# Kernel tuning notes

Hardware: AMD Instinct MI355X
Metric: run time of the kernel (lower is better)

The kernel has to match this reference:

```python
import jax, jax.numpy as jnp
import numpy as np

KAPPA = 0.5  # decorrelation loss mixing coefficient (init kwarg)


def setup_inputs() -> dict:
    key = jax.random.key(0)
    kx, kw, kb, kd, ki = jax.random.split(key, 5)
    b, l, d = 4, 8192, 1024
    n_samples = int(0.25 * l)  # sample_frac = 0.25
    x = jax.random.normal(kx, (b, l, d), dtype=jnp.float32)
    W = jax.random.normal(kw, (d, d), dtype=jnp.float32) * 0.02
    bias = jax.random.normal(kb, (d,), dtype=jnp.float32) * 0.02
    # decorr_layer is initialized at identity in the module; perturb slightly so the
    # decorrelation matmul is non-trivial (it gets updated during training).
    decorr = jnp.eye(d, dtype=jnp.float32) + 0.01 * jax.random.normal(kd, (d, d), dtype=jnp.float32)
    sample_idx = jax.random.randint(ki, (b, n_samples), 0, l)  # stand-in for torch.multinomial
    return {"x": x, "W": W, "bias": bias, "decorr": decorr, "sample_idx": sample_idx}


def reference(x, W, bias, decorr, sample_idx):
    # Output path: y = x @ (W @ decorr)^T + bias
    y = jnp.einsum('bld,od->blo', x, W @ decorr) + bias

    b, l, d = x.shape
    # Gather sampled tokens: [b, n, d]
    selected = jnp.take_along_axis(x, sample_idx[:, :, None], axis=1)
    xs = (selected @ decorr.T).reshape(-1, d)  # [N, d], N = b*n_samples
    N = xs.shape[0]

    # DecorrLoss, algebraically reduced (same math as diag_embed/outer-product form):
    #   C_n = x_n x_n^T - diag(x_n^2)  (zero diagonal, off-diag x_i x_j)
    #   V_n = diag(x_n^2) - I          (diagonal x_i^2 - 1, zero off-diag)
    X2 = xs * xs                     # [N, d]
    m2 = jnp.mean(X2, axis=0)        # [d], mean of x_i^2
    S = X2.T @ X2                    # [d, d]; S_ij = sum_n x_ni^2 x_nj^2
    denom = jnp.float32(N) * d * d
    correlation_loss = (jnp.sum(S) - jnp.trace(S)) / denom       # mean_n mean_ij C_n^2
    whitening_loss = jnp.sum((X2 - 1.0) ** 2) / denom             # mean_n mean_ij V_n^2

    G = (xs.T @ xs) / N              # mean_n x_n x_n^T
    C_mean = G - jnp.diag(m2)
    V_mean = jnp.diag(m2) - jnp.eye(d, dtype=xs.dtype)
    grad = (1.0 - KAPPA) * C_mean + KAPPA * V_mean

    return y, grad, correlation_loss, whitening_loss
```

## Files before the change

### kernel.cpp

```cpp
#include <hip/hip_runtime.h>
#include <cstdint>
#include <cstddef>

typedef __bf16 bf16x8 __attribute__((ext_vector_type(8)));
typedef float  f32x4  __attribute__((ext_vector_type(4)));
typedef unsigned short u16x4 __attribute__((ext_vector_type(4)));

typedef __attribute__((address_space(1))) void* gas1_t;
typedef __attribute__((address_space(3))) void* las3_t;

__device__ __forceinline__ unsigned short f2bf(float f) {
  union { float f; unsigned u; } v; v.f = f;
  unsigned r = v.u + 0x7fffu + ((v.u >> 16) & 1u);
  return (unsigned short)(r >> 16);
}
__device__ __forceinline__ float bf2f(unsigned short h) {
  union { unsigned u; float f; } v; v.u = ((unsigned)h) << 16;
  return v.f;
}

constexpr int Bc = 4, Lc = 8192, Dc = 1024, NSAMP = 2048;
constexpr int ROWS = Bc * Lc;
constexpr int NSEL = Bc * NSAMP;
constexpr long long Y_ELEMS = (long long)ROWS * Dc;
constexpr long long GRAD_OFF = Y_ELEMS;
constexpr long long LOSS_OFF = GRAD_OFF + (long long)Dc*Dc;

constexpr int BM = 128, BN = 128, BK = 64;

template<int MODE>
__global__ void gemm_bt(const unsigned short* __restrict__ A,
                        const unsigned short* __restrict__ B,
                        float* __restrict__ Cf,
                        const float* __restrict__ bias,
                        int M, int N, int K, int kchunk) {
  __shared__ unsigned short sA[BM * BK];
  __shared__ unsigned short sB[BN * BK];
  const int tid  = threadIdx.x;
  const int lane = tid & 63;
  const int wave = tid >> 6;
  const int wm = wave >> 1, wn = wave & 1;
  const int q = lane >> 4, r16 = lane & 15;

  const int gx   = gridDim.x;
  const int nwg  = gx * gridDim.y;
  const int orig = blockIdx.y * gx + blockIdx.x;
  const int swz  = (orig & 7) * (nwg >> 3) + (orig >> 3);
  const int m0 = (swz / gx) * BM;
  const int n0 = (swz % gx) * BN;
  const int kb = blockIdx.z * kchunk;

  const int lrow = lane >> 3;
  const int lcol = (lane & 7) * 8;

  f32x4 acc[4][4] = {};

  for (int k0 = kb; k0 < kb + kchunk; k0 += BK) {
#pragma unroll
    for (int j = 0; j < 4; ++j) {
      const int c = wave * 4 + j;
      const int row = c * 8 + lrow;
      const unsigned short* ga = A + (size_t)(m0 + row) * K + k0 + lcol;
      __builtin_amdgcn_global_load_lds((gas1_t)(void*)ga, (las3_t)(sA + c * 512), 16, 0, 0);
      const unsigned short* gb = B + (size_t)(n0 + row) * K + k0 + lcol;
      __builtin_amdgcn_global_load_lds((gas1_t)(void*)gb, (las3_t)(sB + c * 512), 16, 0, 0);
    }
    __syncthreads();
#pragma unroll
    for (int kk = 0; kk < BK; kk += 32) {
      bf16x8 af[4], bfv[4];
#pragma unroll
      for (int mi = 0; mi < 4; ++mi)
        af[mi] = *(const bf16x8*)(sA + (size_t)(wm*64 + mi*16 + r16) * BK + kk + q*8);
#pragma unroll
      for (int ni = 0; ni < 4; ++ni)
        bfv[ni] = *(const bf16x8*)(sB + (size_t)(wn*64 + ni*16 + r16) * BK + kk + q*8);
#pragma unroll
      for (int mi = 0; mi < 4; ++mi)
#pragma unroll
        for (int ni = 0; ni < 4; ++ni)
          acc[mi][ni] = __builtin_amdgcn_mfma_f32_16x16x32_bf16(af[mi], bfv[ni], acc[mi][ni], 0, 0, 0);
    }
    __syncthreads();
  }

  const int row0 = m0 + wm*64 + q*4;
  const int col0 = n0 + wn*64 + r16;
  float bv[4] = {0.f, 0.f, 0.f, 0.f};
  if (MODE == 0) {
#pragma unroll
    for (int ni = 0; ni < 4; ++ni) bv[ni] = bias[col0 + ni*16];
  }
#pragma unroll
  for (int mi = 0; mi < 4; ++mi) {
#pragma unroll
    for (int r = 0; r < 4; ++r) {
      const int row = row0 + mi*16 + r;
      const size_t base = (size_t)row * N + col0;
#pragma unroll
      for (int ni = 0; ni < 4; ++ni) {
        const size_t o = base + (size_t)ni * 16;
        float v = acc[mi][ni][r];
        if (MODE == 0)      __builtin_nontemporal_store(v + bv[ni], &Cf[o]);
        else if (MODE == 2) Cf[o] = v;
        else                atomicAdd(&Cf[o], v);
      }
    }
  }
}

template<int NT>
__global__ void cvt_f32_bf16(const float* __restrict__ in, unsigned short* __restrict__ out, long long n) {
  long long i = ((long long)blockIdx.x * 256 + threadIdx.x) * 4;
  if (i >= n) return;
  f32x4 v;
  if (NT) v = __builtin_nontemporal_load((const f32x4*)(in + i));
  else    v = *(const f32x4*)(in + i);
  u16x4 o;
  o.x = f2bf(v.x); o.y = f2bf(v.y); o.z = f2bf(v.z); o.w = f2bf(v.w);
  *(u16x4*)(out + i) = o;
}

__global__ void gather_rows(const unsigned short* __restrict__ xb, const int* __restrict__ idx,
                            unsigned short* __restrict__ out) {
  const int blk = blockIdx.x;
  const int b = blk >> 11, n = blk & 2047;
  const int row = idx[b * NSAMP + n];
  const unsigned short* src = xb + ((size_t)b * Lc + row) * Dc;
  unsigned short* dst = out + (size_t)blk * Dc;
  const int c = threadIdx.x * 4;
  *(u16x4*)(dst + c) = *(const u16x4*)(src + c);
}

__global__ void diag_resid(const float* __restrict__ dc, float* __restrict__ cvec) {
  const int i = blockIdx.x * 256 + threadIdx.x;
  if (i >= Dc) return;
  const float v = dc[(size_t)i * Dc + i];
  cvec[i] = v - bf2f(f2bf(v));
}

__global__ void transpose_bf16(const float* __restrict__ in, unsigned short* __restrict__ outT,
                               int R, int C) {
  __shared__ float tile[64][65];
  const int r0 = blockIdx.y * 64, c0 = blockIdx.x * 64;
  const int t = threadIdx.x;
  const int c = t & 63, r4 = t >> 6;
#pragma unroll
  for (int j = 0; j < 16; ++j) {
    const int r = j * 4 + r4;
    tile[r][c] = in[(size_t)(r0 + r) * C + c0 + c];
  }
  __syncthreads();
  const int i = t >> 2, p = t & 3;
  unsigned short* dst = outT + (size_t)(c0 + i) * R + r0 + p * 16;
#pragma unroll
  for (int j = 0; j < 16; j += 4) {
    u16x4 v;
    v.x = f2bf(tile[p*16 + j + 0][i]);
    v.y = f2bf(tile[p*16 + j + 1][i]);
    v.z = f2bf(tile[p*16 + j + 2][i]);
    v.w = f2bf(tile[p*16 + j + 3][i]);
    *(u16x4*)(dst + j) = v;
  }
}

__global__ void xs_stats_transpose(const float* __restrict__ xs, const unsigned short* __restrict__ ab,
                                   const float* __restrict__ cvec,
                                   unsigned short* __restrict__ xsT,
                                   float* __restrict__ m2sum, float* __restrict__ s1g,
                                   float* __restrict__ s2g) {
  __shared__ float tile[64][65];
  const int n0 = blockIdx.x * 64;
  const int i0 = blockIdx.y * 64;
  const int t = threadIdx.x;
  const int c = t & 63, r4 = t >> 6;
  const float ccol = cvec[i0 + c];
#pragma unroll
  for (int j = 0; j < 16; ++j) {
    const int r = j * 4 + r4;
    const size_t o = (size_t)(n0 + r) * Dc + i0 + c;
    tile[r][c] = xs[o] + bf2f(ab[o]) * ccol;
  }
  __syncthreads();
  if (t < 64) {
    float s1 = 0.f, s2 = 0.f;
#pragma unroll
    for (int cc = 0; cc < 64; ++cc) { float v = tile[t][cc]; float v2 = v*v; s1 += v2; s2 += v2*v2; }
    atomicAdd(&s1g[n0 + t], s1);
    atomicAdd(&s2g[n0 + t], s2);
  } else if (t < 128) {
    const int col = t - 64;
    float cs = 0.f;
#pragma unroll
    for (int rr = 0; rr < 64; ++rr) { float v = tile[rr][col]; cs += v*v; }
    atomicAdd(&m2sum[i0 + col], cs);
  }
  const int i = t >> 2, p = t & 3;
  unsigned short* dst = xsT + (size_t)(i0 + i) * NSEL + n0 + p * 16;
#pragma unroll
  for (int j = 0; j < 16; j += 4) {
    u16x4 v;
    v.x = f2bf(tile[p*16 + j + 0][i]);
    v.y = f2bf(tile[p*16 + j + 1][i]);
    v.z = f2bf(tile[p*16 + j + 2][i]);
    v.w = f2bf(tile[p*16 + j + 3][i]);
    *(u16x4*)(dst + j) = v;
  }
}

__global__ void grad_write(const float* __restrict__ G, const float* __restrict__ m2sum,
                           float* __restrict__ out) {
  const int i = blockIdx.x * 256 + threadIdx.x;
  const int r = i >> 10, c = i & 1023;
  float g = G[i] * (0.5f / (float)NSEL);
  if (r == c) g = 0.5f * (m2sum[r] * (1.0f / (float)NSEL) - 1.0f);
  __builtin_nontemporal_store(g, &out[i]);
}

__global__ void finalize_losses(const float* __restrict__ s1g, const float* __restrict__ s2g,
                                float* __restrict__ out2) {
  __shared__ double sa[256], sb[256], sc[256];
  double a = 0, b = 0, c = 0;
  for (int n = threadIdx.x; n < NSEL; n += 256) {
    double s1 = s1g[n], s2 = s2g[n];
    a += s1 * s1; b += s2; c += s1;
  }
  const int t = threadIdx.x;
  sa[t] = a; sb[t] = b; sc[t] = c;
  __syncthreads();
  for (int s = 128; s > 0; s >>= 1) {
    if (t < s) { sa[t] += sa[t+s]; sb[t] += sb[t+s]; sc[t] += sc[t+s]; }
    __syncthreads();
  }
  if (t == 0) {
    const double denom = (double)NSEL * (double)Dc * (double)Dc;
    const double cnt   = (double)NSEL * (double)Dc;
    out2[0] = (float)((sa[0] - sb[0]) / denom);
    out2[1] = (float)((sb[0] - 2.0 * sc[0] + cnt) / denom);
  }
}

extern "C" void kernel_launch(void* const* d_in, const int* in_sizes, int n_in,
                              void* d_out, int out_size, void* d_ws, size_t ws_size,
                              hipStream_t stream) {
  const float* x      = (const float*)d_in[0];
  const float* W      = (const float*)d_in[1];
  const float* bias   = (const float*)d_in[2];
  const float* decorr = (const float*)d_in[3];
  const int*   sidx   = (const int*)d_in[4];
  float* out = (float*)d_out;

  char* w = (char*)d_ws;
  constexpr size_t SZ_XB  = (size_t)ROWS * Dc * 2;
  constexpr size_t SZ_AB  = (size_t)NSEL * Dc * 2;
  constexpr size_t SZ_DT  = (size_t)Dc * Dc * 2;
  constexpr size_t SZ_WB  = (size_t)Dc * Dc * 2;
  constexpr size_t SZ_MB  = (size_t)Dc * Dc * 2;
  constexpr size_t SZ_XS  = (size_t)NSEL * Dc * 4;
  constexpr size_t SZ_XST = (size_t)Dc * NSEL * 2;
  constexpr size_t SZ_MF  = (size_t)Dc * Dc * 4;
  constexpr size_t SZ_GB  = (size_t)Dc * Dc * 4;
  constexpr size_t SZ_M2  = (size_t)Dc * 4;
  constexpr size_t SZ_S1  = (size_t)NSEL * 4;
  constexpr size_t SZ_S2  = (size_t)NSEL * 4;
  constexpr size_t SZ_CV  = (size_t)Dc * 4;

  size_t off = 0;
  unsigned short* xb  = (unsigned short*)(w + off); off += SZ_XB;
  unsigned short* ab  = (unsigned short*)(w + off); off += SZ_AB;
  unsigned short* dT  = (unsigned short*)(w + off); off += SZ_DT;
  unsigned short* wb  = (unsigned short*)(w + off); off += SZ_WB;
  unsigned short* mb  = (unsigned short*)(w + off); off += SZ_MB;
  float*          xsf = (float*)(w + off);          off += SZ_XS;
  unsigned short* xsT = (unsigned short*)(w + off); off += SZ_XST;
  float*          cv  = (float*)(w + off);          off += SZ_CV;
  char*           zbase = w + off;
  float*          Mf  = (float*)(w + off);          off += SZ_MF;
  float*          Gb  = (float*)(w + off);          off += SZ_GB;
  float*          m2s = (float*)(w + off);          off += SZ_M2;
  float*          s1g = (float*)(w + off);          off += SZ_S1;
  float*          s2g = (float*)(w + off);          off += SZ_S2;
  const size_t zbytes = SZ_MF + SZ_GB + SZ_M2 + SZ_S1 + SZ_S2;

  (void)hipMemsetAsync(zbase, 0, zbytes, stream);

  cvt_f32_bf16<1><<<(int)(Y_ELEMS / 1024), 256, 0, stream>>>(x, xb, Y_ELEMS);
  cvt_f32_bf16<0><<<Dc*Dc / 1024, 256, 0, stream>>>(W, wb, (long long)Dc*Dc);
  diag_resid<<<4, 256, 0, stream>>>(decorr, cv);
  transpose_bf16<<<dim3(Dc/64, Dc/64), 256, 0, stream>>>(decorr, dT, Dc, Dc);
  gather_rows<<<NSEL, 256, 0, stream>>>(xb, sidx, ab);

  gemm_bt<3><<<dim3(Dc/BN, Dc/BM, 8), 256, 0, stream>>>(wb, dT, Mf, nullptr, Dc, Dc, Dc, Dc/8);
  cvt_f32_bf16<0><<<Dc*Dc / 1024, 256, 0, stream>>>(Mf, mb, (long long)Dc*Dc);

  gemm_bt<0><<<dim3(Dc/BN, ROWS/BM, 1), 256, 0, stream>>>(xb, mb, out, bias, ROWS, Dc, Dc, Dc);

  gemm_bt<2><<<dim3(Dc/BN, NSEL/BM, 1), 256, 0, stream>>>(ab, dT, xsf, nullptr, NSEL, Dc, Dc, Dc);

  xs_stats_transpose<<<dim3(NSEL/64, Dc/64), 256, 0, stream>>>(xsf, ab, cv, xsT, m2s, s1g, s2g);

  gemm_bt<3><<<dim3(Dc/BN, Dc/BM, 16), 256, 0, stream>>>(xsT, xsT, Gb, nullptr, Dc, Dc, NSEL, NSEL/16);

  grad_write<<<Dc*Dc / 256, 256, 0, stream>>>(Gb, m2s, out + GRAD_OFF);
  finalize_losses<<<1, 256, 0, stream>>>(s1g, s2g, out + LOSS_OFF);
}
```

Before: 470.7 us.

## Add 256x256 direct-to-LDS pipelined GEMM for output and sample projections

Adds a new 512-thread GEMM kernel with 256x256 output tiles. It stages A and B into double-buffered LDS with global_load_lds and splits each K-step into four phases that interleave loads with MFMA bursts under raised wave priority. The main y projection and the sampled-token projection now use this kernel instead of the 128x128 one. The aim is more data reuse per tile and better overlap of memory loads with matrix-core work. In exchange it uses more LDS and registers per block and depends on hand-placed vmcnt waits, and the prologue issues one redundant stage load.

```diff
diff --git a/kernel.cpp b/kernel.cpp
--- a/kernel.cpp
+++ b/kernel.cpp
@@ -25,6 +25,169 @@
 constexpr long long Y_ELEMS = (long long)ROWS * Dc;
 constexpr long long GRAD_OFF = Y_ELEMS;
 constexpr long long LOSS_OFF = GRAD_OFF + (long long)Dc*Dc;
+
+constexpr int BM8 = 256, BN8 = 256;
+
+__device__ __forceinline__ void stage_half(const unsigned short* __restrict__ G,
+                                           unsigned short* lds_half,
+                                           int row0, int K, long long kbase,
+                                           int wave, int srow) {
+#pragma unroll
+  for (int j = 0; j < 2; ++j) {
+    const int w = wave * 2 + j;
+    const unsigned short* src = G + (size_t)(row0 + w * 16 + srow) * K + kbase;
+    __builtin_amdgcn_global_load_lds((gas1_t)(void*)src,
+                                     (las3_t)(lds_half + w * 512), 16, 0, 0);
+  }
+}
+
+__device__ __forceinline__ void ld4(const unsigned short* base, int l8, bf16x8* dst) {
+#pragma unroll
+  for (int i = 0; i < 4; ++i)
+    dst[i] = *(const bf16x8*)(base + i * 512 + l8);
+}
+
+#define PH_WAIT() do {                                        \
+    __builtin_amdgcn_s_barrier();                             \
+    asm volatile("s_waitcnt lgkmcnt(0)" ::: "memory");        \
+    __builtin_amdgcn_sched_barrier(0);                        \
+  } while (0)
+
+template<int MODE>
+__global__ __launch_bounds__(512, 2)
+void gemm_bt8(const unsigned short* __restrict__ A,
+              const unsigned short* __restrict__ B,
+              float* __restrict__ Cf,
+              const float* __restrict__ bias,
+              int M, int N, int K) {
+  __shared__ unsigned short sA[2 * 16384];
+  __shared__ unsigned short sB[2 * 16384];
+  const int tid  = threadIdx.x;
+  const int lane = tid & 63;
+  const int wave = tid >> 6;
+  const int wm = wave >> 2;
+  const int wn = wave & 3;
+  const int q = lane >> 4, r16 = lane & 15;
+  const int l8 = lane * 8;
+  const int srow = lane & 15;
+  const long long scol = (lane >> 4) * 8;
+
+  const int gx   = gridDim.x;
+  const int nwg  = gx * gridDim.y;
+  const int orig = blockIdx.y * gx + blockIdx.x;
+  const int swz  = (orig & 7) * (nwg >> 3) + (orig >> 3);
+  const int m0 = (swz / gx) * BM8;
+  const int n0 = (swz % gx) * BN8;
+
+  const int nt = K >> 6;
+
+  f32x4 acc[8][4] = {};
+
+  {
+    stage_half(A, sA + 0 * 16384 + 0 * 8192, m0, K, 0,            wave, srow ? srow : srow);
+  }
+  stage_half(A, sA + 0,          m0, K, 0 * 64 + 0 * 32 + scol, wave, srow);
+  stage_half(A, sA + 8192,       m0, K, 0 * 64 + 1 * 32 + scol, wave, srow);
+  stage_half(B, sB + 0,          n0, K, 0 * 64 + 0 * 32 + scol, wave, srow);
+  stage_half(B, sB + 8192,       n0, K, 0 * 64 + 1 * 32 + scol, wave, srow);
+  if (nt > 1) {
+    stage_half(B, sB + 16384 + 0,    n0, K, 1 * 64 + 0 * 32 + scol, wave, srow);
+    stage_half(A, sA + 16384 + 0,    m0, K, 1 * 64 + 0 * 32 + scol, wave, srow);
+    stage_half(B, sB + 16384 + 8192, n0, K, 1 * 64 + 1 * 32 + scol, wave, srow);
+    asm volatile("s_waitcnt vmcnt(6)" ::: "memory");
+  } else {
+    asm volatile("s_waitcnt vmcnt(0)" ::: "memory");
+  }
+  __builtin_amdgcn_s_barrier();
+
+  for (int g = 0; g < nt; ++g) {
+    const int buf = (g & 1) * 16384;
+    const int nbuf = 16384 - buf;
+    bf16x8 af[4], bfv[4];
+
+    ld4(sA + buf + (wm * 8 + 0) * 512, l8, af);
+    ld4(sB + buf + (wn * 4)     * 512, l8, bfv);
+    if (g + 1 < nt)
+      stage_half(A, sA + nbuf + 8192, m0, K, (long long)(g + 1) * 64 + 32 + scol, wave, srow);
+    PH_WAIT();
+    __builtin_amdgcn_s_setprio(1);
+#pragma unroll
+    for (int i = 0; i < 4; ++i)
+#pragma unroll
+      for (int ni = 0; ni < 4; ++ni)
+        acc[i][ni] = __builtin_amdgcn_mfma_f32_16x16x32_bf16(af[i], bfv[ni], acc[i][ni], 0, 0, 0);
+    __builtin_amdgcn_s_setprio(0);
+    __builtin_amdgcn_s_barrier();
+
+    ld4(sA + buf + (wm * 8 + 4) * 512, l8, af);
+    if (g + 2 < nt)
+      stage_half(B, sB + buf, n0, K, (long long)(g + 2) * 64 + scol, wave, srow);
+    PH_WAIT();
+    __builtin_amdgcn_s_setprio(1);
+#pragma unroll
+    for (int i = 0; i < 4; ++i)
+#pragma unroll
+      for (int ni = 0; ni < 4; ++ni)
+        acc[4 + i][ni] = __builtin_amdgcn_mfma_f32_16x16x32_bf16(af[i], bfv[ni], acc[4 + i][ni], 0, 0, 0);
+    __builtin_amdgcn_s_setprio(0);
+    __builtin_amdgcn_s_barrier();
+
+    ld4(sA + buf + 8192 + (wm * 8 + 0) * 512, l8, af);
+    ld4(sB + buf + 8192 + (wn * 4)     * 512, l8, bfv);
+    if (g + 2 < nt)
+      stage_half(A, sA + buf, m0, K, (long long)(g + 2) * 64 + scol, wave, srow);
+    PH_WAIT();
+    __builtin_amdgcn_s_setprio(1);
+#pragma unroll
+    for (int i = 0; i < 4; ++i)
+#pragma unroll
+      for (int ni = 0; ni < 4; ++ni)
+        acc[i][ni] = __builtin_amdgcn_mfma_f32_16x16x32_bf16(af[i], bfv[ni], acc[i][ni], 0, 0, 0);
+    __builtin_amdgcn_s_setprio(0);
+    __builtin_amdgcn_s_barrier();
+
+    ld4(sA + buf + 8192 + (wm * 8 + 4) * 512, l8, af);
+    if (g + 2 < nt)
+      stage_half(B, sB + buf + 8192, n0, K, (long long)(g + 2) * 64 + 32 + scol, wave, srow);
+    PH_WAIT();
+    __builtin_amdgcn_s_setprio(1);
+#pragma unroll
+    for (int i = 0; i < 4; ++i)
+#pragma unroll
+      for (int ni = 0; ni < 4; ++ni)
+        acc[4 + i][ni] = __builtin_amdgcn_mfma_f32_16x16x32_bf16(af[i], bfv[ni], acc[4 + i][ni], 0, 0, 0);
+    __builtin_amdgcn_s_setprio(0);
+
+    if (g + 1 < nt) {
+      if (g + 2 < nt) asm volatile("s_waitcnt vmcnt(6)" ::: "memory");
+      else            asm volatile("s_waitcnt vmcnt(0)" ::: "memory");
+    }
+    __builtin_amdgcn_s_barrier();
+  }
+
+  const int row0 = m0 + wm * 128 + q * 4;
+  const int col0 = n0 + wn * 64 + r16;
+  float bv[4] = {0.f, 0.f, 0.f, 0.f};
+  if (MODE == 0) {
+#pragma unroll
+    for (int ni = 0; ni < 4; ++ni) bv[ni] = bias[col0 + ni * 16];
+  }
+#pragma unroll
+  for (int mi = 0; mi < 8; ++mi) {
+#pragma unroll
+    for (int r = 0; r < 4; ++r) {
+      const int row = row0 + mi * 16 + r;
+      const size_t base = (size_t)row * N + col0;
+#pragma unroll
+      for (int ni = 0; ni < 4; ++ni) {
+        const size_t o = base + (size_t)ni * 16;
+        float v = acc[mi][ni][r];
+        if (MODE == 0) __builtin_nontemporal_store(v + bv[ni], &Cf[o]);
+        else           Cf[o] = v;
+      }
+    }
+  }
+}
 
 constexpr int BM = 128, BN = 128, BK = 64;
 
@@ -293,9 +456,9 @@
   gemm_bt<3><<<dim3(Dc/BN, Dc/BM, 8), 256, 0, stream>>>(wb, dT, Mf, nullptr, Dc, Dc, Dc, Dc/8);
   cvt_f32_bf16<0><<<Dc*Dc / 1024, 256, 0, stream>>>(Mf, mb, (long long)Dc*Dc);
 
-  gemm_bt<0><<<dim3(Dc/BN, ROWS/BM, 1), 256, 0, stream>>>(xb, mb, out, bias, ROWS, Dc, Dc, Dc);
-
-  gemm_bt<2><<<dim3(Dc/BN, NSEL/BM, 1), 256, 0, stream>>>(ab, dT, xsf, nullptr, NSEL, Dc, Dc, Dc);
+  gemm_bt8<0><<<dim3(Dc/BN8, ROWS/BM8), 512, 0, stream>>>(xb, mb, out, bias, ROWS, Dc, Dc);
+
+  gemm_bt8<2><<<dim3(Dc/BN8, NSEL/BM8), 512, 0, stream>>>(ab, dT, xsf, nullptr, NSEL, Dc, Dc);
 
   xs_stats_transpose<<<dim3(NSEL/64, Dc/64), 256, 0, stream>>>(xsf, ab, cv, xsT, m2s, s1g, s2g);
 
```

Measured after the change: 503.9 us. 1.07x slower.

## Fuse xs GEMM with stats/transpose epilogue and exploit Gram symmetry

Applied to the files above, without the earlier changes.

Folds the sampled-token GEMM together with the diagonal residual correction, per-row and per-column square sums, and bf16 transpose into one kernel. This removes the fp32 xs round trip and a separate kernel. The Gram GEMM computes only the upper-triangular 128x128 tiles, and grad_write mirrors them. W conversion, decorr transpose and the diagonal residual are merged into one prep kernel, and the W@decorr GEMM writes bf16 directly without split-K atomics. The loss statistics are now computed from bf16-rounded xs values, which slightly changes precision.

```diff
diff --git a/kernel.cpp b/kernel.cpp
--- a/kernel.cpp
+++ b/kernel.cpp
@@ -42,12 +42,19 @@
   const int wm = wave >> 1, wn = wave & 1;
   const int q = lane >> 4, r16 = lane & 15;
 
-  const int gx   = gridDim.x;
-  const int nwg  = gx * gridDim.y;
-  const int orig = blockIdx.y * gx + blockIdx.x;
-  const int swz  = (orig & 7) * (nwg >> 3) + (orig >> 3);
-  const int m0 = (swz / gx) * BM;
-  const int n0 = (swz % gx) * BN;
+  int m0, n0;
+  if constexpr (MODE == 6) {
+    int t = blockIdx.x, ti = 0;
+    while (t >= 8 - ti) { t -= 8 - ti; ++ti; }
+    m0 = ti * BM; n0 = (ti + t) * BN;
+  } else {
+    const int gx   = gridDim.x;
+    const int nwg  = gx * gridDim.y;
+    const int orig = blockIdx.y * gx + blockIdx.x;
+    const int swz  = (orig & 7) * (nwg >> 3) + (orig >> 3);
+    m0 = (swz / gx) * BM;
+    n0 = (swz % gx) * BN;
+  }
   const int kb = blockIdx.z * kchunk;
 
   const int lrow = lane >> 3;
@@ -102,10 +109,121 @@
         const size_t o = base + (size_t)ni * 16;
         float v = acc[mi][ni][r];
         if (MODE == 0)      __builtin_nontemporal_store(v + bv[ni], &Cf[o]);
-        else if (MODE == 2) Cf[o] = v;
+        else if (MODE == 5) ((unsigned short*)Cf)[o] = f2bf(v);
         else                atomicAdd(&Cf[o], v);
       }
     }
+  }
+}
+
+__global__ __launch_bounds__(256)
+void xs_gemm_fused(const unsigned short* __restrict__ A,
+                   const unsigned short* __restrict__ B,
+                   const float* __restrict__ cvec,
+                   unsigned short* __restrict__ xsT,
+                   float* __restrict__ m2sum, float* __restrict__ s1g,
+                   float* __restrict__ s2g,
+                   int M, int N, int K) {
+  __shared__ __attribute__((aligned(16))) unsigned short shm[128 * 136];
+  unsigned short* sA = shm;
+  unsigned short* sB = shm + 8192;
+  const int tid  = threadIdx.x;
+  const int lane = tid & 63;
+  const int wave = tid >> 6;
+  const int wm = wave >> 1, wn = wave & 1;
+  const int q = lane >> 4, r16 = lane & 15;
+
+  const int gx   = gridDim.x;
+  const int nwg  = gx * gridDim.y;
+  const int orig = blockIdx.y * gx + blockIdx.x;
+  const int swz  = (orig & 7) * (nwg >> 3) + (orig >> 3);
+  const int m0 = (swz / gx) * BM;
+  const int n0 = (swz % gx) * BN;
+
+  const int lrow = lane >> 3;
+  const int lcol = (lane & 7) * 8;
+
+  f32x4 acc[4][4] = {};
+
+  for (int k0 = 0; k0 < K; k0 += BK) {
+#pragma unroll
+    for (int j = 0; j < 4; ++j) {
+      const int c = wave * 4 + j;
+      const int row = c * 8 + lrow;
+      const unsigned short* ga = A + (size_t)(m0 + row) * K + k0 + lcol;
+      __builtin_amdgcn_global_load_lds((gas1_t)(void*)ga, (las3_t)(sA + c * 512), 16, 0, 0);
+      const unsigned short* gb = B + (size_t)(n0 + row) * K + k0 + lcol;
+      __builtin_amdgcn_global_load_lds((gas1_t)(void*)gb, (las3_t)(sB + c * 512), 16, 0, 0);
+    }
+    __syncthreads();
+#pragma unroll
+    for (int kk = 0; kk < BK; kk += 32) {
+      bf16x8 af[4], bfv[4];
+#pragma unroll
+      for (int mi = 0; mi < 4; ++mi)
+        af[mi] = *(const bf16x8*)(sA + (size_t)(wm*64 + mi*16 + r16) * BK + kk + q*8);
+#pragma unroll
+      for (int ni = 0; ni < 4; ++ni)
+        bfv[ni] = *(const bf16x8*)(sB + (size_t)(wn*64 + ni*16 + r16) * BK + kk + q*8);
+#pragma unroll
+      for (int mi = 0; mi < 4; ++mi)
+#pragma unroll
+        for (int ni = 0; ni < 4; ++ni)
+          acc[mi][ni] = __builtin_amdgcn_mfma_f32_16x16x32_bf16(af[mi], bfv[ni], acc[mi][ni], 0, 0, 0);
+    }
+    __syncthreads();
+  }
+
+  const int lr0 = wm*64 + q*4;
+  const int lc0 = wn*64 + r16;
+  float cvl[4];
+#pragma unroll
+  for (int ni = 0; ni < 4; ++ni) cvl[ni] = cvec[n0 + lc0 + ni*16];
+#pragma unroll
+  for (int mi = 0; mi < 4; ++mi) {
+#pragma unroll
+    for (int r = 0; r < 4; ++r) {
+      const int lr = lr0 + mi*16 + r;
+      const size_t arow = (size_t)(m0 + lr) * K;
+#pragma unroll
+      for (int ni = 0; ni < 4; ++ni) {
+        const int lc = lc0 + ni*16;
+        float v = acc[mi][ni][r] + bf2f(A[arow + n0 + lc]) * cvl[ni];
+        shm[lr * 136 + lc] = f2bf(v);
+      }
+    }
+  }
+  __syncthreads();
+
+  if (tid < 128) {
+    float s1 = 0.f, s2 = 0.f;
+#pragma unroll 8
+    for (int c = 0; c < 128; ++c) {
+      float v = bf2f(shm[tid * 136 + c]); float v2 = v * v;
+      s1 += v2; s2 += v2 * v2;
+    }
+    atomicAdd(&s1g[m0 + tid], s1);
+    atomicAdd(&s2g[m0 + tid], s2);
+  } else {
+    const int col = tid - 128;
+    float cs = 0.f;
+#pragma unroll 8
+    for (int r = 0; r < 128; ++r) {
+      float v = bf2f(shm[r * 136 + col]); cs += v * v;
+    }
+    atomicAdd(&m2sum[n0 + col], cs);
+  }
+
+  const int fi = tid >> 1, hh = tid & 1;
+  unsigned short* dst = xsT + (size_t)(n0 + fi) * M + m0 + hh * 64;
+#pragma unroll
+  for (int j = 0; j < 64; j += 4) {
+    u16x4 v;
+    v.x = shm[(hh*64 + j + 0) * 136 + fi];
+    v.y = shm[(hh*64 + j + 1) * 136 + fi];
+    v.z = shm[(hh*64 + j + 2) * 136 + fi];
+    v.w = shm[(hh*64 + j + 3) * 136 + fi];
+    *(u16x4*)(dst + j) = v;
   }
 }
 
@@ -132,15 +250,9 @@
   *(u16x4*)(dst + c) = *(const u16x4*)(src + c);
 }
 
-__global__ void diag_resid(const float* __restrict__ dc, float* __restrict__ cvec) {
-  const int i = blockIdx.x * 256 + threadIdx.x;
-  if (i >= Dc) return;
-  const float v = dc[(size_t)i * Dc + i];
-  cvec[i] = v - bf2f(f2bf(v));
-}
-
-__global__ void transpose_bf16(const float* __restrict__ in, unsigned short* __restrict__ outT,
-                               int R, int C) {
+__global__ void prep_wdt(const float* __restrict__ W, const float* __restrict__ dc,
+                         unsigned short* __restrict__ wb, unsigned short* __restrict__ dT,
+                         float* __restrict__ cvec) {
   __shared__ float tile[64][65];
   const int r0 = blockIdx.y * 64, c0 = blockIdx.x * 64;
   const int t = threadIdx.x;
@@ -148,11 +260,17 @@
 #pragma unroll
   for (int j = 0; j < 16; ++j) {
     const int r = j * 4 + r4;
-    tile[r][c] = in[(size_t)(r0 + r) * C + c0 + c];
+    const size_t o = (size_t)(r0 + r) * Dc + c0 + c;
+    wb[o] = f2bf(W[o]);
+    tile[r][c] = dc[o];
   }
   __syncthreads();
+  if (blockIdx.x == blockIdx.y && t < 64) {
+    const float v = tile[t][t];
+    cvec[c0 + t] = v - bf2f(f2bf(v));
+  }
   const int i = t >> 2, p = t & 3;
-  unsigned short* dst = outT + (size_t)(c0 + i) * R + r0 + p * 16;
+  unsigned short* dst = dT + (size_t)(c0 + i) * Dc + r0 + p * 16;
 #pragma unroll
   for (int j = 0; j < 16; j += 4) {
     u16x4 v;
@@ -164,55 +282,13 @@
   }
 }
 
-__global__ void xs_stats_transpose(const float* __restrict__ xs, const unsigned short* __restrict__ ab,
-                                   const float* __restrict__ cvec,
-                                   unsigned short* __restrict__ xsT,
-                                   float* __restrict__ m2sum, float* __restrict__ s1g,
-                                   float* __restrict__ s2g) {
-  __shared__ float tile[64][65];
-  const int n0 = blockIdx.x * 64;
-  const int i0 = blockIdx.y * 64;
-  const int t = threadIdx.x;
-  const int c = t & 63, r4 = t >> 6;
-  const float ccol = cvec[i0 + c];
-#pragma unroll
-  for (int j = 0; j < 16; ++j) {
-    const int r = j * 4 + r4;
-    const size_t o = (size_t)(n0 + r) * Dc + i0 + c;
-    tile[r][c] = xs[o] + bf2f(ab[o]) * ccol;
-  }
-  __syncthreads();
-  if (t < 64) {
-    float s1 = 0.f, s2 = 0.f;
-#pragma unroll
-    for (int cc = 0; cc < 64; ++cc) { float v = tile[t][cc]; float v2 = v*v; s1 += v2; s2 += v2*v2; }
-    atomicAdd(&s1g[n0 + t], s1);
-    atomicAdd(&s2g[n0 + t], s2);
-  } else if (t < 128) {
-    const int col = t - 64;
-    float cs = 0.f;
-#pragma unroll
-    for (int rr = 0; rr < 64; ++rr) { float v = tile[rr][col]; cs += v*v; }
-    atomicAdd(&m2sum[i0 + col], cs);
-  }
-  const int i = t >> 2, p = t & 3;
-  unsigned short* dst = xsT + (size_t)(i0 + i) * NSEL + n0 + p * 16;
-#pragma unroll
-  for (int j = 0; j < 16; j += 4) {
-    u16x4 v;
-    v.x = f2bf(tile[p*16 + j + 0][i]);
-    v.y = f2bf(tile[p*16 + j + 1][i]);
-    v.z = f2bf(tile[p*16 + j + 2][i]);
-    v.w = f2bf(tile[p*16 + j + 3][i]);
-    *(u16x4*)(dst + j) = v;
-  }
-}
-
 __global__ void grad_write(const float* __restrict__ G, const float* __restrict__ m2sum,
                            float* __restrict__ out) {
   const int i = blockIdx.x * 256 + threadIdx.x;
   const int r = i >> 10, c = i & 1023;
-  float g = G[i] * (0.5f / (float)NSEL);
+  int rr = r, cc = c;
+  if ((r >> 7) > (c >> 7)) { rr = c; cc = r; }
+  float g = G[rr * 1024 + cc] * (0.5f / (float)NSEL);
   if (r == c) g = 0.5f * (m2sum[r] * (1.0f / (float)NSEL) - 1.0f);
   __builtin_nontemporal_store(g, &out[i]);
 }
@@ -256,14 +332,12 @@
   constexpr size_t SZ_DT  = (size_t)Dc * Dc * 2;
   constexpr size_t SZ_WB  = (size_t)Dc * Dc * 2;
   constexpr size_t SZ_MB  = (size_t)Dc * Dc * 2;
-  constexpr size_t SZ_XS  = (size_t)NSEL * Dc * 4;
   constexpr size_t SZ_XST = (size_t)Dc * NSEL * 2;
-  constexpr size_t SZ_MF  = (size_t)Dc * Dc * 4;
+  constexpr size_t SZ_CV  = (size_t)Dc * 4;
   constexpr size_t SZ_GB  = (size_t)Dc * Dc * 4;
   constexpr size_t SZ_M2  = (size_t)Dc * 4;
   constexpr size_t SZ_S1  = (size_t)NSEL * 4;
   constexpr size_t SZ_S2  = (size_t)NSEL * 4;
-  constexpr size_t SZ_CV  = (size_t)Dc * 4;
 
   size_t off = 0;
   unsigned short* xb  = (unsigned short*)(w + off); off += SZ_XB;
@@ -271,35 +345,29 @@
   unsigned short* dT  = (unsigned short*)(w + off); off += SZ_DT;
   unsigned short* wb  = (unsigned short*)(w + off); off += SZ_WB;
   unsigned short* mb  = (unsigned short*)(w + off); off += SZ_MB;
-  float*          xsf = (float*)(w + off);          off += SZ_XS;
   unsigned short* xsT = (unsigned short*)(w + off); off += SZ_XST;
   float*          cv  = (float*)(w + off);          off += SZ_CV;
   char*           zbase = w + off;
-  float*          Mf  = (float*)(w + off);          off += SZ_MF;
   float*          Gb  = (float*)(w + off);          off += SZ_GB;
   float*          m2s = (float*)(w + off);          off += SZ_M2;
   float*          s1g = (float*)(w + off);          off += SZ_S1;
   float*          s2g = (float*)(w + off);          off += SZ_S2;
-  const size_t zbytes = SZ_MF + SZ_GB + SZ_M2 + SZ_S1 + SZ_S2;
+  const size_t zbytes = SZ_GB + SZ_M2 + SZ_S1 + SZ_S2;
 
   (void)hipMemsetAsync(zbase, 0, zbytes, stream);
 
   cvt_f32_bf16<1><<<(int)(Y_ELEMS / 1024), 256, 0, stream>>>(x, xb, Y_ELEMS);
-  cvt_f32_bf16<0><<<Dc*Dc / 1024, 256, 0, stream>>>(W, wb, (long long)Dc*Dc);
-  diag_resid<<<4, 256, 0, stream>>>(decorr, cv);
-  transpose_bf16<<<dim3(Dc/64, Dc/64), 256, 0, stream>>>(decorr, dT, Dc, Dc);
+  prep_wdt<<<dim3(16, 16), 256, 0, stream>>>(W, decorr, wb, dT, cv);
   gather_rows<<<NSEL, 256, 0, stream>>>(xb, sidx, ab);
 
-  gemm_bt<3><<<dim3(Dc/BN, Dc/BM, 8), 256, 0, stream>>>(wb, dT, Mf, nullptr, Dc, Dc, Dc, Dc/8);
-  cvt_f32_bf16<0><<<Dc*Dc / 1024, 256, 0, stream>>>(Mf, mb, (long long)Dc*Dc);
+  gemm_bt<5><<<dim3(Dc/BN, Dc/BM, 1), 256, 0, stream>>>(wb, dT, (float*)mb, nullptr, Dc, Dc, Dc, Dc);
 
   gemm_bt<0><<<dim3(Dc/BN, ROWS/BM, 1), 256, 0, stream>>>(xb, mb, out, bias, ROWS, Dc, Dc, Dc);
 
-  gemm_bt<2><<<dim3(Dc/BN, NSEL/BM, 1), 256, 0, stream>>>(ab, dT, xsf, nullptr, NSEL, Dc, Dc, Dc);
-
-  xs_stats_transpose<<<dim3(NSEL/64, Dc/64), 256, 0, stream>>>(xsf, ab, cv, xsT, m2s, s1g, s2g);
-
-  gemm_bt<3><<<dim3(Dc/BN, Dc/BM, 16), 256, 0, stream>>>(xsT, xsT, Gb, nullptr, Dc, Dc, NSEL, NSEL/16);
+  xs_gemm_fused<<<dim3(Dc/BN, NSEL/BM), 256, 0, stream>>>(ab, dT, cv, xsT, m2s, s1g, s2g,
+                                                          NSEL, Dc, Dc);
+
+  gemm_bt<6><<<dim3(36, 1, 8), 256, 0, stream>>>(xsT, xsT, Gb, nullptr, Dc, Dc, NSEL, NSEL/8);
 
   grad_write<<<Dc*Dc / 256, 256, 0, stream>>>(Gb, m2s, out + GRAD_OFF);
   finalize_losses<<<1, 256, 0, stream>>>(s1g, s2g, out + LOSS_OFF);
```

Measured after the change: 422.5 us. -10.3%, faster.
